# Performance work log

Hardware: AMD Instinct MI355X
Metric: run time of the kernel (lower is better)

## Reference

```python
import jax, jax.numpy as jnp
import numpy as np
from jax import lax

B, N_SITES, FEAT, BOND, OUT = 2048, 128, 64, 32, 256
CORE_SCALE = 0.02  # keeps the 128-step matrix product finite


def setup_inputs() -> dict:
    key = jax.random.key(0)
    ks = jax.random.split(key, 6)
    return {
        "x": jax.random.normal(ks[0], (B, N_SITES, FEAT), dtype=jnp.float32),
        "cores": jax.random.normal(ks[1], (N_SITES, BOND, FEAT, BOND), dtype=jnp.float32) * CORE_SCALE,
        "start": jax.random.normal(ks[2], (1, BOND), dtype=jnp.float32),
        "end": jax.random.normal(ks[3], (BOND, 1), dtype=jnp.float32),
        "fc_w": jax.random.normal(ks[4], (OUT, 1), dtype=jnp.float32),
        "fc_b": jax.random.normal(ks[5], (OUT,), dtype=jnp.float32),
    }


def reference(x, cores, start, end, fc_w, fc_b):
    # x: [B, N, F]; cores: [N, D, F, D]; start: [1, D]; end: [D, 1]
    b = x.shape[0]
    res0 = jnp.broadcast_to(start, (b, start.shape[1]))  # [B, D]

    def step(res, site):
        xi, core = site  # xi: [B, F], core: [D, F, D]
        m = jnp.einsum('bf,dfr->bdr', xi, core)  # per-site transfer matrix [B, D, D]
        return jnp.einsum('bd,bdr->br', res, m), None

    res, _ = lax.scan(step, res0, (jnp.swapaxes(x, 0, 1), cores))
    val = res @ end  # [B, 1]
    return val @ fc_w.T + fc_b  # [B, OUT]
```

## Files before the change

### kernel.cpp

```cpp
#include <hip/hip_runtime.h>


#define NSITES 128
#define FEATD  64
#define BOND   32
#define OUTD   256
#define BT     16
#define SEGLEN 16
#define NSEG   (NSITES / SEGLEN)
#define NBT    (2048 / BT)

#define RSTRIDE 48
#define BSTRIDE 1552

typedef __attribute__((ext_vector_type(4))) float float4v;

__device__ __forceinline__ unsigned pk4_fp8(float a, float b, float c, float d) {
    int v = __builtin_amdgcn_cvt_pk_fp8_f32(a, b, 0, false);
    v = __builtin_amdgcn_cvt_pk_fp8_f32(c, d, v, true);
    return (unsigned)v;
}

__global__ __launch_bounds__(256)
void prep_cores8(const float* __restrict__ cores, unsigned char* __restrict__ core8) {
    __shared__ float tile[FEATD][BOND + 4];
    const int nd = blockIdx.x;
    const int t  = threadIdx.x;
    const float* src = cores + (size_t)nd * (FEATD * BOND);
    {
        int base = t * 8;
        int f = base >> 5, r0 = base & 31;
        float4 v0 = *(const float4*)(src + base);
        float4 v1 = *(const float4*)(src + base + 4);
        tile[f][r0 + 0] = v0.x; tile[f][r0 + 1] = v0.y;
        tile[f][r0 + 2] = v0.z; tile[f][r0 + 3] = v0.w;
        tile[f][r0 + 4] = v1.x; tile[f][r0 + 5] = v1.y;
        tile[f][r0 + 6] = v1.z; tile[f][r0 + 7] = v1.w;
    }
    __syncthreads();
    const int r = t >> 3, f0 = (t & 7) * 8;
    const float s = 16.0f;
    unsigned lo = pk4_fp8(tile[f0 + 0][r] * s, tile[f0 + 1][r] * s,
                          tile[f0 + 2][r] * s, tile[f0 + 3][r] * s);
    unsigned hi = pk4_fp8(tile[f0 + 4][r] * s, tile[f0 + 5][r] * s,
                          tile[f0 + 6][r] * s, tile[f0 + 7][r] * s);
    uint2 w; w.x = lo; w.y = hi;
    *(uint2*)(core8 + ((size_t)nd * BOND + r) * FEATD + f0) = w;
}

__global__ __launch_bounds__(512, 4)
void mps_seg(const float* __restrict__ x, const unsigned char* __restrict__ core8,
             unsigned char* __restrict__ Pout) {
    __shared__ __align__(16) unsigned char MS[BT * BSTRIDE];
    __shared__ __align__(16) unsigned char PS[BT * BSTRIDE];
    __shared__ __align__(16) unsigned char XS[BT * 72];

    const int t    = threadIdx.x;
    const int wave = t >> 6;
    const int lane = t & 63;
    const int cl   = lane & 15;
    const int q    = lane >> 4;
    const int bt   = blockIdx.x;
    const int seg  = blockIdx.y;
    const int b0   = bt * BT;

    {
        int b = t >> 5, d = t & 31;
        unsigned w[8];
#pragma unroll
        for (int dw = 0; dw < 8; ++dw)
            w[dw] = ((d >> 2) == dw) ? (0x58u << ((d & 3) * 8)) : 0u;
        uint4* p = (uint4*)&PS[b * BSTRIDE + d * RSTRIDE];
        p[0] = make_uint4(w[0], w[1], w[2], w[3]);
        p[1] = make_uint4(w[4], w[5], w[6], w[7]);
    }

    const int xb = t >> 5, xf = (t & 31) * 2;
    float2 xf2 = *(const float2*)(x + ((size_t)(b0 + xb) * NSITES + seg * SEGLEN) * FEATD + xf);

    for (int k = 0; k < SEGLEN; ++k) {
        const int n = seg * SEGLEN + k;

        long af[16];
        {
            const unsigned char* base = core8 + (size_t)n * (1024 * FEATD);
#pragma unroll
            for (int i = 0; i < 8; ++i) {
                const unsigned char* p =
                    base + (size_t)((wave * 8 + i) * 16 + cl) * FEATD + q * 8;
                af[i * 2 + 0] = *(const long*)p;
                af[i * 2 + 1] = *(const long*)(p + 32);
            }
        }

        {
            int v = __builtin_amdgcn_cvt_pk_fp8_f32(xf2.x, xf2.y, 0, false);
            *(unsigned short*)&XS[xb * 72 + xf] = (unsigned short)(v & 0xffff);
        }
        __syncthreads();

        long bx0 = *(const long*)&XS[cl * 72 + q * 8];
        long bx1 = *(const long*)&XS[cl * 72 + 32 + q * 8];
        float4v acc[8];
#pragma unroll
        for (int i = 0; i < 8; ++i) {
            float4v z = {0.f, 0.f, 0.f, 0.f};
            z = __builtin_amdgcn_mfma_f32_16x16x32_fp8_fp8(af[i * 2 + 0], bx0, z, 0, 0, 0);
            acc[i] = __builtin_amdgcn_mfma_f32_16x16x32_fp8_fp8(af[i * 2 + 1], bx1, z, 0, 0, 0);
        }

#pragma unroll
        for (int p = 0; p < 2; ++p)
#pragma unroll
            for (int g = 0; g < 4; ++g) {
                unsigned w = pk4_fp8(acc[0 + p][g], acc[2 + p][g],
                                     acc[4 + p][g], acc[6 + p][g]);
                *(unsigned*)&MS[cl * BSTRIDE + (16 * p + 4 * q + g) * RSTRIDE + wave * 4] = w;
            }

        if (k + 1 < SEGLEN)
            xf2 = *(const float2*)(x + ((size_t)(b0 + xb) * NSITES + n + 1) * FEATD + xf);

        __syncthreads();

        long pa[2][2], pb[2][2];
#pragma unroll
        for (int bi = 0; bi < 2; ++bi) {
            int bb = wave * 2 + bi;
#pragma unroll
            for (int h = 0; h < 2; ++h) {
                pa[bi][h] = *(const long*)&MS[bb * BSTRIDE + (h * 16 + cl) * RSTRIDE + q * 8];
                pb[bi][h] = *(const long*)&PS[bb * BSTRIDE + (h * 16 + cl) * RSTRIDE + q * 8];
            }
        }
        float4v pacc[2][2][2];
#pragma unroll
        for (int bi = 0; bi < 2; ++bi)
#pragma unroll
            for (int I = 0; I < 2; ++I)
#pragma unroll
                for (int J = 0; J < 2; ++J) {
                    float4v z = {0.f, 0.f, 0.f, 0.f};
                    pacc[bi][I][J] =
                        __builtin_amdgcn_mfma_f32_16x16x32_fp8_fp8(pa[bi][I], pb[bi][J], z, 0, 0, 0);
                }
#pragma unroll
        for (int bi = 0; bi < 2; ++bi) {
            int bb = wave * 2 + bi;
#pragma unroll
            for (int I = 0; I < 2; ++I)
#pragma unroll
                for (int J = 0; J < 2; ++J) {
                    float4v c = pacc[bi][I][J];
                    unsigned w = pk4_fp8(c[0] * 0.0625f, c[1] * 0.0625f,
                                         c[2] * 0.0625f, c[3] * 0.0625f);
                    *(unsigned*)&PS[bb * BSTRIDE + (J * 16 + cl) * RSTRIDE + I * 16 + q * 4] = w;
                }
        }
    }

    __syncthreads();
    {
        int b = t >> 5, d = t & 31;
        const uint4* p = (const uint4*)&PS[b * BSTRIDE + d * RSTRIDE];
        uint4* g = (uint4*)(Pout + (((size_t)seg * 2048 + b0 + b) * 1024 + d * 32));
        g[0] = p[0];
        g[1] = p[1];
    }
}

__global__ __launch_bounds__(256)
void combine(const unsigned char* __restrict__ Pout, const float* __restrict__ startv,
             const float* __restrict__ endv, const float* __restrict__ fc_w,
             const float* __restrict__ fc_b, float* __restrict__ out) {
    __shared__ __align__(16) unsigned char st[8 * 1024];
    __shared__ float resA[8][33], resB[8][33];
    __shared__ float val[8];
    const int t  = threadIdx.x;
    const int b0 = blockIdx.x * 8;
    const int bb = t >> 5, r = t & 31;

    resA[bb][r] = startv[r];
    for (int s = 0; s < NSEG; ++s) {
        {
            const uint4* g = (const uint4*)(Pout + ((size_t)s * 2048 + b0) * 1024 + (size_t)t * 32);
            uint4* p = (uint4*)&st[t * 32];
            p[0] = g[0];
            p[1] = g[1];
        }
        __syncthreads();
        const float* rin = (s & 1) ? &resB[bb][0] : &resA[bb][0];
        float* rout      = (s & 1) ? &resA[bb][0] : &resB[bb][0];
        float acc = 0.f;
#pragma unroll
        for (int d = 0; d < BOND; ++d) {
            int byte = st[bb * 1024 + d * 32 + r];
            acc += rin[d] * __builtin_amdgcn_cvt_f32_fp8(byte, 0);
        }
        rout[r] = acc * 0.0625f;
        __syncthreads();
    }
    float prod = resA[bb][r] * endv[r];
#pragma unroll
    for (int off = 16; off >= 1; off >>= 1) prod += __shfl_down(prod, off, 32);
    if (r == 0) val[bb] = prod;
    __syncthreads();

    const float v = val[t >> 5];
    const int j0 = (t & 31) * 8;
    const int ob = b0 + (t >> 5);
#pragma unroll
    for (int i = 0; i < 2; ++i) {
        int j = j0 + i * 4;
        float4 w4 = *(const float4*)(fc_w + j);
        float4 bbv = *(const float4*)(fc_b + j);
        float4 o;
        o.x = v * w4.x + bbv.x;
        o.y = v * w4.y + bbv.y;
        o.z = v * w4.z + bbv.z;
        o.w = v * w4.w + bbv.w;
        *(float4*)(out + (size_t)ob * OUTD + j) = o;
    }
}

extern "C" void kernel_launch(void* const* d_in, const int* in_sizes, int n_in,
                              void* d_out, int out_size, void* d_ws, size_t ws_size,
                              hipStream_t stream) {
    const float* x      = (const float*)d_in[0];
    const float* cores  = (const float*)d_in[1];
    const float* startv = (const float*)d_in[2];
    const float* endv   = (const float*)d_in[3];
    const float* fc_w   = (const float*)d_in[4];
    const float* fc_b   = (const float*)d_in[5];
    float* out = (float*)d_out;

    unsigned char* core8 = (unsigned char*)d_ws;
    unsigned char* Pout  = core8 + (size_t)NSITES * 1024 * FEATD;

    prep_cores8<<<NSITES * BOND, 256, 0, stream>>>(cores, core8);
    mps_seg<<<dim3(NBT, NSEG), 512, 0, stream>>>(x, core8, Pout);
    combine<<<2048 / 8, 256, 0, stream>>>(Pout, startv, endv, fc_w, fc_b, out);
}
```

Before: 243.5 us.

## Keep running segment product in registers via bpermute and restructure combine kernel

The per-batch running product matrix is now held in registers and its C-layout is remapped into the MFMA B-operand layout with ds_bpermute, which removes the PS shared buffer and its LDS store/load round trip. With half the LDS per block, launch bounds are raised to 8 blocks per SM. Core loads are split into two halves to lower register pressure, and the x prefetch is moved earlier. The combine kernel is rewritten to use one wave per batch with shuffles and prefetched bytes instead of shared memory and block barriers, at the cost of many scattered byte loads.

```diff
diff --git a/kernel.cpp b/kernel.cpp
--- a/kernel.cpp
+++ b/kernel.cpp
@@ -48,11 +48,10 @@
     *(uint2*)(core8 + ((size_t)nd * BOND + r) * FEATD + f0) = w;
 }
 
-__global__ __launch_bounds__(512, 4)
+__global__ __launch_bounds__(512, 8)
 void mps_seg(const float* __restrict__ x, const unsigned char* __restrict__ core8,
              unsigned char* __restrict__ Pout) {
     __shared__ __align__(16) unsigned char MS[BT * BSTRIDE];
-    __shared__ __align__(16) unsigned char PS[BT * BSTRIDE];
     __shared__ __align__(16) unsigned char XS[BT * 72];
 
     const int t    = threadIdx.x;
@@ -60,167 +59,175 @@
     const int lane = t & 63;
     const int cl   = lane & 15;
     const int q    = lane >> 4;
-    const int bt   = blockIdx.x;
+    const int b0   = blockIdx.x * BT;
     const int seg  = blockIdx.y;
-    const int b0   = bt * BT;
-
-    {
-        int b = t >> 5, d = t & 31;
-        unsigned w[8];
-#pragma unroll
-        for (int dw = 0; dw < 8; ++dw)
-            w[dw] = ((d >> 2) == dw) ? (0x58u << ((d & 3) * 8)) : 0u;
-        uint4* p = (uint4*)&PS[b * BSTRIDE + d * RSTRIDE];
-        p[0] = make_uint4(w[0], w[1], w[2], w[3]);
-        p[1] = make_uint4(w[4], w[5], w[6], w[7]);
-    }
+
+    int pw[2][2][2];
+#pragma unroll
+    for (int bi = 0; bi < 2; ++bi)
+#pragma unroll
+        for (int I = 0; I < 2; ++I)
+#pragma unroll
+            for (int J = 0; J < 2; ++J) {
+                int v = 0;
+                int g = cl - 4 * q;
+                if (I == J && g >= 0 && g < 4) v = 0x58 << (g * 8);
+                pw[bi][I][J] = v;
+            }
 
     const int xb = t >> 5, xf = (t & 31) * 2;
     float2 xf2 = *(const float2*)(x + ((size_t)(b0 + xb) * NSITES + seg * SEGLEN) * FEATD + xf);
+    {
+        int v = __builtin_amdgcn_cvt_pk_fp8_f32(xf2.x, xf2.y, 0, false);
+        *(unsigned short*)&XS[xb * 72 + xf] = (unsigned short)(v & 0xffff);
+    }
+
+    const int hi32  = (lane & 32) ? 1 : 0;
+    const int addr0 = (cl + ((lane & 16) << 1)) * 4;
+    const int addr1 = addr0 + 64;
 
     for (int k = 0; k < SEGLEN; ++k) {
         const int n = seg * SEGLEN + k;
-
-        long af[16];
-        {
-            const unsigned char* base = core8 + (size_t)n * (1024 * FEATD);
-#pragma unroll
-            for (int i = 0; i < 8; ++i) {
-                const unsigned char* p =
-                    base + (size_t)((wave * 8 + i) * 16 + cl) * FEATD + q * 8;
-                af[i * 2 + 0] = *(const long*)p;
-                af[i * 2 + 1] = *(const long*)(p + 32);
-            }
-        }
-
-        {
-            int v = __builtin_amdgcn_cvt_pk_fp8_f32(xf2.x, xf2.y, 0, false);
-            *(unsigned short*)&XS[xb * 72 + xf] = (unsigned short)(v & 0xffff);
-        }
         __syncthreads();
 
+        const unsigned char* cbase = core8 + (size_t)n * (1024 * FEATD);
         long bx0 = *(const long*)&XS[cl * 72 + q * 8];
         long bx1 = *(const long*)&XS[cl * 72 + 32 + q * 8];
-        float4v acc[8];
-#pragma unroll
-        for (int i = 0; i < 8; ++i) {
-            float4v z = {0.f, 0.f, 0.f, 0.f};
-            z = __builtin_amdgcn_mfma_f32_16x16x32_fp8_fp8(af[i * 2 + 0], bx0, z, 0, 0, 0);
-            acc[i] = __builtin_amdgcn_mfma_f32_16x16x32_fp8_fp8(af[i * 2 + 1], bx1, z, 0, 0, 0);
-        }
-
-#pragma unroll
-        for (int p = 0; p < 2; ++p)
+
+        float2 xn;
+        if (k + 1 < SEGLEN)
+            xn = *(const float2*)(x + ((size_t)(b0 + xb) * NSITES + n + 1) * FEATD + xf);
+
+#pragma unroll
+        for (int p = 0; p < 2; ++p) {
+            long afA[4], afB[4];
+#pragma unroll
+            for (int u = 0; u < 4; ++u) {
+                const unsigned char* ptr =
+                    cbase + (size_t)((wave * 8 + 2 * u + p) * 16 + cl) * FEATD + q * 8;
+                afA[u] = *(const long*)ptr;
+                afB[u] = *(const long*)(ptr + 32);
+            }
+            float4v acc[4];
+#pragma unroll
+            for (int u = 0; u < 4; ++u) {
+                float4v z = {0.f, 0.f, 0.f, 0.f};
+                z = __builtin_amdgcn_mfma_f32_16x16x32_fp8_fp8(afA[u], bx0, z, 0, 0, 0);
+                acc[u] = __builtin_amdgcn_mfma_f32_16x16x32_fp8_fp8(afB[u], bx1, z, 0, 0, 0);
+            }
 #pragma unroll
             for (int g = 0; g < 4; ++g) {
-                unsigned w = pk4_fp8(acc[0 + p][g], acc[2 + p][g],
-                                     acc[4 + p][g], acc[6 + p][g]);
+                unsigned w = pk4_fp8(acc[0][g], acc[1][g], acc[2][g], acc[3][g]);
                 *(unsigned*)&MS[cl * BSTRIDE + (16 * p + 4 * q + g) * RSTRIDE + wave * 4] = w;
             }
-
-        if (k + 1 < SEGLEN)
-            xf2 = *(const float2*)(x + ((size_t)(b0 + xb) * NSITES + n + 1) * FEATD + xf);
+        }
 
         __syncthreads();
 
-        long pa[2][2], pb[2][2];
 #pragma unroll
         for (int bi = 0; bi < 2; ++bi) {
-            int bb = wave * 2 + bi;
+            const int bb = wave * 2 + bi;
+            long pa0 = *(const long*)&MS[bb * BSTRIDE + (0 * 16 + cl) * RSTRIDE + q * 8];
+            long pa1 = *(const long*)&MS[bb * BSTRIDE + (1 * 16 + cl) * RSTRIDE + q * 8];
+            long pbv[2];
 #pragma unroll
             for (int h = 0; h < 2; ++h) {
-                pa[bi][h] = *(const long*)&MS[bb * BSTRIDE + (h * 16 + cl) * RSTRIDE + q * 8];
-                pb[bi][h] = *(const long*)&PS[bb * BSTRIDE + (h * 16 + cl) * RSTRIDE + q * 8];
-            }
-        }
-        float4v pacc[2][2][2];
-#pragma unroll
-        for (int bi = 0; bi < 2; ++bi)
+                int l0a = __builtin_amdgcn_ds_bpermute(addr0, pw[bi][0][h]);
+                int l0b = __builtin_amdgcn_ds_bpermute(addr0, pw[bi][1][h]);
+                int l1a = __builtin_amdgcn_ds_bpermute(addr1, pw[bi][0][h]);
+                int l1b = __builtin_amdgcn_ds_bpermute(addr1, pw[bi][1][h]);
+                int d0 = hi32 ? l0b : l0a;
+                int d1 = hi32 ? l1b : l1a;
+                pbv[h] = ((long)(unsigned)d0) | (((long)d1) << 32);
+            }
+            float4v pc[2][2];
 #pragma unroll
             for (int I = 0; I < 2; ++I)
 #pragma unroll
                 for (int J = 0; J < 2; ++J) {
                     float4v z = {0.f, 0.f, 0.f, 0.f};
-                    pacc[bi][I][J] =
-                        __builtin_amdgcn_mfma_f32_16x16x32_fp8_fp8(pa[bi][I], pb[bi][J], z, 0, 0, 0);
+                    pc[I][J] = __builtin_amdgcn_mfma_f32_16x16x32_fp8_fp8(
+                        I ? pa1 : pa0, pbv[J], z, 0, 0, 0);
                 }
 #pragma unroll
-        for (int bi = 0; bi < 2; ++bi) {
-            int bb = wave * 2 + bi;
-#pragma unroll
             for (int I = 0; I < 2; ++I)
 #pragma unroll
-                for (int J = 0; J < 2; ++J) {
-                    float4v c = pacc[bi][I][J];
-                    unsigned w = pk4_fp8(c[0] * 0.0625f, c[1] * 0.0625f,
-                                         c[2] * 0.0625f, c[3] * 0.0625f);
-                    *(unsigned*)&PS[bb * BSTRIDE + (J * 16 + cl) * RSTRIDE + I * 16 + q * 4] = w;
-                }
-        }
-    }
-
-    __syncthreads();
-    {
-        int b = t >> 5, d = t & 31;
-        const uint4* p = (const uint4*)&PS[b * BSTRIDE + d * RSTRIDE];
-        uint4* g = (uint4*)(Pout + (((size_t)seg * 2048 + b0 + b) * 1024 + d * 32));
-        g[0] = p[0];
-        g[1] = p[1];
-    }
-}
-
-__global__ __launch_bounds__(256)
+                for (int J = 0; J < 2; ++J)
+                    pw[bi][I][J] = (int)pk4_fp8(pc[I][J][0] * 0.0625f, pc[I][J][1] * 0.0625f,
+                                                pc[I][J][2] * 0.0625f, pc[I][J][3] * 0.0625f);
+        }
+
+        if (k + 1 < SEGLEN) {
+            int v = __builtin_amdgcn_cvt_pk_fp8_f32(xn.x, xn.y, 0, false);
+            *(unsigned short*)&XS[xb * 72 + xf] = (unsigned short)(v & 0xffff);
+        }
+    }
+
+#pragma unroll
+    for (int bi = 0; bi < 2; ++bi) {
+        const int bb = wave * 2 + bi;
+        unsigned char* gp = Pout + (((size_t)seg * 2048 + b0 + bb) * 1024);
+#pragma unroll
+        for (int I = 0; I < 2; ++I)
+#pragma unroll
+            for (int J = 0; J < 2; ++J)
+                *(unsigned*)(gp + (J * 16 + cl) * 32 + I * 16 + q * 4) =
+                    (unsigned)pw[bi][I][J];
+    }
+}
+
+__global__ __launch_bounds__(512)
 void combine(const unsigned char* __restrict__ Pout, const float* __restrict__ startv,
              const float* __restrict__ endv, const float* __restrict__ fc_w,
              const float* __restrict__ fc_b, float* __restrict__ out) {
-    __shared__ __align__(16) unsigned char st[8 * 1024];
-    __shared__ float resA[8][33], resB[8][33];
-    __shared__ float val[8];
-    const int t  = threadIdx.x;
-    const int b0 = blockIdx.x * 8;
-    const int bb = t >> 5, r = t & 31;
-
-    resA[bb][r] = startv[r];
+    const int t    = threadIdx.x;
+    const int wave = t >> 6;
+    const int lane = t & 63;
+    const int r    = lane >> 1;
+    const int dh   = lane & 1;
+    const int b    = blockIdx.x * 8 + wave;
+
+    float res = startv[r];
+    const unsigned char* base = Pout + (size_t)b * 1024 + dh * 512 + r;
+
+    unsigned char by[16];
+#pragma unroll
+    for (int di = 0; di < 16; ++di) by[di] = base[di * 32];
+
     for (int s = 0; s < NSEG; ++s) {
-        {
-            const uint4* g = (const uint4*)(Pout + ((size_t)s * 2048 + b0) * 1024 + (size_t)t * 32);
-            uint4* p = (uint4*)&st[t * 32];
-            p[0] = g[0];
-            p[1] = g[1];
-        }
-        __syncthreads();
-        const float* rin = (s & 1) ? &resB[bb][0] : &resA[bb][0];
-        float* rout      = (s & 1) ? &resA[bb][0] : &resB[bb][0];
+        unsigned char by2[16];
+        if (s + 1 < NSEG) {
+            const unsigned char* nb = base + (size_t)(s + 1) * 2048 * 1024;
+#pragma unroll
+            for (int di = 0; di < 16; ++di) by2[di] = nb[di * 32];
+        }
         float acc = 0.f;
 #pragma unroll
-        for (int d = 0; d < BOND; ++d) {
-            int byte = st[bb * 1024 + d * 32 + r];
-            acc += rin[d] * __builtin_amdgcn_cvt_f32_fp8(byte, 0);
-        }
-        rout[r] = acc * 0.0625f;
-        __syncthreads();
-    }
-    float prod = resA[bb][r] * endv[r];
-#pragma unroll
-    for (int off = 16; off >= 1; off >>= 1) prod += __shfl_down(prod, off, 32);
-    if (r == 0) val[bb] = prod;
-    __syncthreads();
-
-    const float v = val[t >> 5];
-    const int j0 = (t & 31) * 8;
-    const int ob = b0 + (t >> 5);
-#pragma unroll
-    for (int i = 0; i < 2; ++i) {
-        int j = j0 + i * 4;
-        float4 w4 = *(const float4*)(fc_w + j);
-        float4 bbv = *(const float4*)(fc_b + j);
-        float4 o;
-        o.x = v * w4.x + bbv.x;
-        o.y = v * w4.y + bbv.y;
-        o.z = v * w4.z + bbv.z;
-        o.w = v * w4.w + bbv.w;
-        *(float4*)(out + (size_t)ob * OUTD + j) = o;
-    }
+        for (int di = 0; di < 16; ++di) {
+            float rv = __shfl(res, dh * 32 + di * 2, 64);
+            acc += rv * __builtin_amdgcn_cvt_f32_fp8((int)by[di], 0);
+        }
+        float tot = acc + __shfl_xor(acc, 1, 64);
+        res = tot * 0.0625f;
+        if (s + 1 < NSEG) {
+#pragma unroll
+            for (int di = 0; di < 16; ++di) by[di] = by2[di];
+        }
+    }
+
+    float v = dh ? 0.f : res * endv[r];
+#pragma unroll
+    for (int off = 1; off < 64; off <<= 1) v += __shfl_xor(v, off, 64);
+
+    const int j = lane * 4;
+    float4 w4  = *(const float4*)(fc_w + j);
+    float4 bb4 = *(const float4*)(fc_b + j);
+    float4 o;
+    o.x = v * w4.x + bb4.x;
+    o.y = v * w4.y + bb4.y;
+    o.z = v * w4.z + bb4.z;
+    o.w = v * w4.w + bb4.w;
+    *(float4*)(out + (size_t)b * OUTD + j) = o;
 }
 
 extern "C" void kernel_launch(void* const* d_in, const int* in_sizes, int n_in,
@@ -239,5 +246,5 @@
 
     prep_cores8<<<NSITES * BOND, 256, 0, stream>>>(cores, core8);
     mps_seg<<<dim3(NBT, NSEG), 512, 0, stream>>>(x, core8, Pout);
-    combine<<<2048 / 8, 256, 0, stream>>>(Pout, startv, endv, fc_w, fc_b, out);
-}
+    combine<<<2048 / 8, 512, 0, stream>>>(Pout, startv, endv, fc_w, fc_b, out);
+}
```

Result: slower. 266.1 us (+9.3%).
